# Kernel tuning notes

Measured on AMD Instinct MI355X. Metric: run time of the kernel, lower is better.

The kernel has to match this reference:

```python
import jax, jax.numpy as jnp
import numpy as np

B, Q, L, D = 4, 600, 2048, 256
H, HD, DFF, KD = 8, 32, 2048, 32  # heads, head_dim, ffn dim, gasa kernel dim
SCALE = HD ** -0.5


def setup_inputs() -> dict:
    key = jax.random.key(0)
    ks = jax.random.split(key, 24)
    w = lambda k, shape, s=0.02: (jax.random.normal(k, shape, jnp.float32) * s)
    inp = {
        "queries": jax.random.normal(ks[0], (B, Q, D), jnp.float32),
        "memory": jax.random.normal(ks[1], (B, L, D), jnp.float32),
        "memory_pos": jax.random.normal(ks[2], (B, L, 3), jnp.float32),
        "query_pos": jax.random.normal(ks[3], (B, Q, 3), jnp.float32),
        # self-attention (nn.MultiheadAttention packed in_proj)
        "sa_in_w": w(ks[4], (3 * D, D)), "sa_in_b": jnp.zeros((3 * D,), jnp.float32),
        "sa_out_w": w(ks[5], (D, D)), "sa_out_b": jnp.zeros((D,), jnp.float32),
        "norm1_g": jnp.ones((D,), jnp.float32), "norm1_b": jnp.zeros((D,), jnp.float32),
        # cross-attention projections
        "q_w": w(ks[6], (D, D)), "q_b": jnp.zeros((D,), jnp.float32),
        "k_w": w(ks[7], (D, D)), "k_b": jnp.zeros((D,), jnp.float32),
        "v_w": w(ks[8], (D, D)), "v_b": jnp.zeros((D,), jnp.float32),
        "o_w": w(ks[9], (D, D)), "o_b": jnp.zeros((D,), jnp.float32),
        "norm2_g": jnp.ones((D,), jnp.float32), "norm2_b": jnp.zeros((D,), jnp.float32),
        # GASA geometric-bias kernel: beta, MLP 1->KD->1
        "beta": jnp.asarray(1.0, jnp.float32),
        "dk_w1": w(ks[10], (KD, 1), 0.1), "dk_b1": jnp.zeros((KD,), jnp.float32),
        "dk_w2": w(ks[11], (1, KD), 0.1), "dk_b2": jnp.full((1,), -1.0, jnp.float32),
        # FFN
        "ffn_w1": w(ks[12], (DFF, D)), "ffn_b1": jnp.zeros((DFF,), jnp.float32),
        "ffn_w2": w(ks[13], (D, DFF)), "ffn_b2": jnp.zeros((D,), jnp.float32),
        "norm3_g": jnp.ones((D,), jnp.float32), "norm3_b": jnp.zeros((D,), jnp.float32),
    }
    return inp


def _ln(x, g, b, eps=1e-5):
    m = jnp.mean(x, -1, keepdims=True)
    v = jnp.mean((x - m) ** 2, -1, keepdims=True)
    return (x - m) * jax.lax.rsqrt(v + eps) * g + b


def _heads(x, wt, b):  # x:[B,N,D] -> [B,H,N,HD]
    y = x @ wt.T + b
    return y.reshape(x.shape[0], x.shape[1], H, HD).transpose(0, 2, 1, 3)


def reference(queries, memory, memory_pos, query_pos,
              sa_in_w, sa_in_b, sa_out_w, sa_out_b, norm1_g, norm1_b,
              q_w, q_b, k_w, k_b, v_w, v_b, o_w, o_b, norm2_g, norm2_b,
              beta, dk_w1, dk_b1, dk_w2, dk_b2,
              ffn_w1, ffn_b1, ffn_w2, ffn_b2, norm3_g, norm3_b):
    # ---- self-attention (post-norm, no query_pe) ----
    wq, wk, wv = jnp.split(sa_in_w, 3, axis=0)
    bq, bk, bv = jnp.split(sa_in_b, 3)
    qh = _heads(queries, wq, bq)
    kh = _heads(queries, wk, bk)
    vh = _heads(queries, wv, bv)
    a = jax.nn.softmax(jnp.einsum('bhqd,bhkd->bhqk', qh, kh) * SCALE, axis=-1)
    sa = jnp.einsum('bhqk,bhkd->bhqd', a, vh).transpose(0, 2, 1, 3).reshape(B, Q, D)
    sa = sa @ sa_out_w.T + sa_out_b
    x = _ln(queries + sa, norm1_g, norm1_b)

    # ---- GASA cross-attention ----
    Qh = _heads(x, q_w, q_b)          # [B,H,Q,HD]
    Kh = _heads(memory, k_w, k_b)     # [B,H,L,HD]
    Vh = _heads(memory, v_w, v_b)     # [B,H,L,HD]
    # cdist + learned kernel MLP, clamp to [-10, 0] (suppress-only)
    d2 = jnp.sum((query_pos[:, :, None, :] - memory_pos[:, None, :, :]) ** 2, -1)
    dist = jnp.sqrt(jnp.maximum(d2, 0.0))                     # [B,Q,L]
    hid = jax.nn.relu(dist[..., None] * dk_w1[:, 0] + dk_b1)  # [B,Q,L,KD]
    bias = (hid @ dk_w2[0]) + dk_b2[0]                        # [B,Q,L]
    bias = jnp.clip(bias, -10.0, 0.0)
    scores = jnp.einsum('bhqd,bhkd->bhqk', Qh, Kh) * SCALE + beta * bias[:, None]
    attn = jax.nn.softmax(scores, axis=-1)
    ca = jnp.einsum('bhqk,bhkd->bhqd', attn, Vh).transpose(0, 2, 1, 3).reshape(B, Q, D)
    ca = ca @ o_w.T + o_b
    x = _ln(x + ca, norm2_g, norm2_b)

    # ---- FFN (post-norm) ----
    f = jax.nn.relu(x @ ffn_w1.T + ffn_b1) @ ffn_w2.T + ffn_b2
    return _ln(x + f, norm3_g, norm3_b)
```

## Files before the change

### kernel.cpp

```cpp
#include <hip/hip_runtime.h>
#include <hip/hip_bf16.h>

typedef __hip_bfloat16 bf16;
typedef __attribute__((ext_vector_type(8))) short  short8;
typedef __attribute__((ext_vector_type(4))) short  short4v;
typedef __attribute__((ext_vector_type(4))) float  f32x4;

#define B_ 4
#define Q_ 600
#define L_ 2048
#define D_ 256
#define H_ 8
#define HD_ 32
#define DFF_ 2048
#define KD_ 32
#define SCALE_ 0.17677669529663687f
#define L2E_   1.4426950408889634f
#define SL2E_  (SCALE_ * L2E_)

template<int MODE>
__device__ __forceinline__ float ldx(const void* p, size_t i, bool f32)
{
    if (MODE == 0) return __bfloat162float(((const bf16*)p)[i]);
    if (MODE == 1) return ((const float*)p)[i];
    return f32 ? ((const float*)p)[i] : __bfloat162float(((const bf16*)p)[i]);
}
__device__ __forceinline__ short8 ld8_f32(const float* p)
{
    const float4 a = *(const float4*)p;
    const float4 b = *(const float4*)(p + 4);
    union { short8 s; bf16 h[8]; } u;
    u.h[0] = __float2bfloat16(a.x); u.h[1] = __float2bfloat16(a.y);
    u.h[2] = __float2bfloat16(a.z); u.h[3] = __float2bfloat16(a.w);
    u.h[4] = __float2bfloat16(b.x); u.h[5] = __float2bfloat16(b.y);
    u.h[6] = __float2bfloat16(b.z); u.h[7] = __float2bfloat16(b.w);
    return u.s;
}
template<int MODE>
__device__ __forceinline__ short8 ld8x(const void* p, size_t i, bool f32)
{
    if (MODE == 0) return *(const short8*)((const bf16*)p + i);
    if (MODE == 1) return ld8_f32((const float*)p + i);
    return f32 ? ld8_f32((const float*)p + i) : *(const short8*)((const bf16*)p + i);
}

template<int NSEG>
__device__ __forceinline__ short8 ld8_comb(const bf16* __restrict__ pO,
                                           const float* __restrict__ pml,
                                           int row, int col)
{
    const unsigned b = (unsigned)row / 600u;
    const unsigned q = (unsigned)row - b * 600u;
    const int h = col >> 5, dd = col & 31;
    const unsigned rp = b * 4800u + (unsigned)h * 600u + q;
    float W = 0.f;
    float acc[8] = {0.f,0.f,0.f,0.f,0.f,0.f,0.f,0.f};
    #pragma unroll
    for (int s = 0; s < NSEG; s++) {
        const size_t rr = (size_t)s * 19200u + rp;
        const float l = pml[rr * 2 + 1];
        W += l;
        const short8 o = *(const short8*)(pO + rr * 32 + dd);
        #pragma unroll
        for (int j = 0; j < 8; j++)
            acc[j] += l * __bfloat162float(((const bf16*)&o)[j]);
    }
    const float inv = 1.f / W;
    union { short8 s; bf16 h8[8]; } u;
    #pragma unroll
    for (int j = 0; j < 8; j++) u.h8[j] = __float2bfloat16(acc[j] * inv);
    return u.s;
}

__global__ __launch_bounds__(256)
void detect_kernel(const unsigned short* __restrict__ q, int* __restrict__ flag)
{
    __shared__ float red[4];
    const int tid = threadIdx.x;
    unsigned short u = q[tid];
    float f = __uint_as_float(((unsigned)(u & 0x7FFF)) << 16);
    if (f != f) f = 1e30f;
    #pragma unroll
    for (int o = 32; o > 0; o >>= 1) f = fmaxf(f, __shfl_xor(f, o));
    if ((tid & 63) == 0) red[tid >> 6] = f;
    __syncthreads();
    if (tid == 0) {
        float m = fmaxf(fmaxf(red[0], red[1]), fmaxf(red[2], red[3]));
        *flag = (m > 100.f) ? 1 : 0;
    }
}

template<int AM, int NSEG>
__device__ __forceinline__ void gemm_core(const void* __restrict__ A,
    const void* __restrict__ W, int M, int K, int kbeg, int kend,
    int bm, int bn, bool f32, bf16* As, bf16* Bs, f32x4 (&acc)[2][2],
    const float* __restrict__ pml)
{
    const int tid = threadIdx.x;
    const int w = tid >> 6, lane = tid & 63;
    const int quad = lane >> 4, l16 = lane & 15;
    const int wm = (w & 1) << 5, wn = (w >> 1) << 5;
    const int srow = tid >> 2, scol = (tid & 3) << 3;
    const int gma = (bm + srow < M) ? bm + srow : M - 1;

    short8 pa, pb;
    if constexpr (AM == 3) pa = ld8_comb<NSEG>((const bf16*)A, pml, gma, kbeg + scol);
    else                   pa = ld8x<AM>(A, (size_t)gma * K + kbeg + scol, f32);
    pb = ld8x<2>(W, (size_t)(bn + srow) * K + kbeg + scol, f32);

    for (int k0 = kbeg; k0 < kend; k0 += 32) {
        *(short8*)&As[srow * 40 + scol] = pa;
        *(short8*)&Bs[srow * 40 + scol] = pb;
        __syncthreads();
        if (k0 + 32 < kend) {
            if constexpr (AM == 3) pa = ld8_comb<NSEG>((const bf16*)A, pml, gma, k0 + 32 + scol);
            else                   pa = ld8x<AM>(A, (size_t)gma * K + k0 + 32 + scol, f32);
            pb = ld8x<2>(W, (size_t)(bn + srow) * K + k0 + 32 + scol, f32);
        }
        short8 af[2], bfr[2];
        #pragma unroll
        for (int t = 0; t < 2; t++) {
            af[t]  = *(const short8*)&As[(wm + t * 16 + l16) * 40 + quad * 8];
            bfr[t] = *(const short8*)&Bs[(wn + t * 16 + l16) * 40 + quad * 8];
        }
        #pragma unroll
        for (int mt = 0; mt < 2; mt++)
            #pragma unroll
            for (int nt = 0; nt < 2; nt++)
                acc[mt][nt] = __builtin_amdgcn_mfma_f32_16x16x32_bf16(
                    af[mt], bfr[nt], acc[mt][nt], 0, 0, 0);
        __syncthreads();
    }
}

template<int RM, int CM, bool RELU>
__device__ __forceinline__ void gemm_epi(const f32x4 (&acc)[2][2],
    const void* __restrict__ bias, const void* __restrict__ R,
    void* __restrict__ C, int M, int N, int bm, int bn, bool f32)
{
    const int tid = threadIdx.x;
    const int w = tid >> 6, lane = tid & 63;
    const int quad = lane >> 4, l16 = lane & 15;
    const int wm = (w & 1) << 5, wn = (w >> 1) << 5;
    #pragma unroll
    for (int mt = 0; mt < 2; mt++) {
        #pragma unroll
        for (int r = 0; r < 4; r++) {
            const int row = bm + wm + mt * 16 + quad * 4 + r;
            if (row >= M) continue;
            #pragma unroll
            for (int nt = 0; nt < 2; nt++) {
                const int col = bn + wn + nt * 16 + l16;
                float v = acc[mt][nt][r] + ldx<2>(bias, col, f32);
                if (RM >= 0) v += ldx<(RM < 0 ? 0 : RM)>(R, (size_t)row * N + col, f32);
                if (RELU) v = fmaxf(v, 0.f);
                if (CM == 0) ((bf16*)C)[(size_t)row * N + col] = __float2bfloat16(v);
                else         ((float*)C)[(size_t)row * N + col] = v;
            }
        }
    }
}

template<int AM, int RM, int CM, bool RELU, int SPLIT, int NSEG>
__global__ __launch_bounds__(256)
void gemm_mfma(const void* __restrict__ A, const void* __restrict__ W,
               const void* __restrict__ bias, const void* __restrict__ R,
               void* __restrict__ C, int M, int N, int K,
               const int* __restrict__ flagp, const float* __restrict__ pml)
{
    const bool f32 = (*flagp != 0);
    __shared__ alignas(16) bf16 As[64 * 40];
    __shared__ alignas(16) bf16 Bs[64 * 40];
    const int bm = blockIdx.y << 6, bn = blockIdx.x << 6;
    const int KS = K / SPLIT, z = (SPLIT > 1) ? blockIdx.z : 0;

    f32x4 acc[2][2] = {{{0.f,0.f,0.f,0.f},{0.f,0.f,0.f,0.f}},
                       {{0.f,0.f,0.f,0.f},{0.f,0.f,0.f,0.f}}};
    gemm_core<AM, NSEG>(A, W, M, K, z * KS, z * KS + KS, bm, bn, f32, As, Bs, acc, pml);

    if (SPLIT > 1) {
        const int tid = threadIdx.x;
        const int w = tid >> 6, lane = tid & 63;
        const int quad = lane >> 4, l16 = lane & 15;
        const int wm = (w & 1) << 5, wn = (w >> 1) << 5;
        #pragma unroll
        for (int mt = 0; mt < 2; mt++)
            #pragma unroll
            for (int r = 0; r < 4; r++) {
                const int row = bm + wm + mt * 16 + quad * 4 + r;
                if (row >= M) continue;
                #pragma unroll
                for (int nt = 0; nt < 2; nt++) {
                    const int col = bn + wn + nt * 16 + l16;
                    ((float*)C)[((size_t)z * M + row) * N + col] = acc[mt][nt][r];
                }
            }
    } else {
        gemm_epi<RM, CM, RELU>(acc, bias, R, C, M, N, bm, bn, f32);
    }
}

__global__ __launch_bounds__(256)
void kv_proj(const void* __restrict__ A,
             const void* __restrict__ kw, const void* __restrict__ kb,
             const void* __restrict__ vw, const void* __restrict__ vb,
             bf16* __restrict__ kf, bf16* __restrict__ vf,
             int M, int K, const int* __restrict__ flagp)
{
    const bool f32 = (*flagp != 0);
    __shared__ alignas(16) bf16 As[64 * 40];
    __shared__ alignas(16) bf16 Bs[64 * 40];
    const int sel = blockIdx.x >> 2;
    const void* W  = sel ? vw : kw;
    const void* bs = sel ? vb : kb;
    bf16* C        = sel ? vf : kf;
    const int bn = (blockIdx.x & 3) << 6;
    const int bm = blockIdx.y << 6;

    f32x4 acc[2][2] = {{{0.f,0.f,0.f,0.f},{0.f,0.f,0.f,0.f}},
                       {{0.f,0.f,0.f,0.f},{0.f,0.f,0.f,0.f}}};
    gemm_core<2, 1>(A, W, M, K, 0, K, bm, bn, f32, As, Bs, acc, nullptr);
    gemm_epi<-1, 0, false>(acc, bs, nullptr, C, M, 256, bm, bn, f32);
}

__global__ __launch_bounds__(256)
void bias_pre(const void* __restrict__ qp, const void* __restrict__ mp,
              const void* __restrict__ w1, const void* __restrict__ b1,
              const void* __restrict__ w2, const void* __restrict__ b2,
              const void* __restrict__ betap, bf16* __restrict__ out,
              const int* __restrict__ flagp)
{
    const bool f32 = (*flagp != 0);
    __shared__ float sw1[KD_], sb1[KD_], sw2[KD_], scst[2];
    const int tid = threadIdx.x;
    if (tid < KD_) {
        sw1[tid] = ldx<2>(w1, tid, f32);
        sb1[tid] = ldx<2>(b1, tid, f32);
        sw2[tid] = ldx<2>(w2, tid, f32);
    }
    if (tid == 0) { scst[0] = ldx<2>(b2, 0, f32); scst[1] = L2E_ * ldx<2>(betap, 0, f32); }
    __syncthreads();
    const int idx = blockIdx.x * 256 + tid;
    const int q8 = idx % 75;
    const int t2 = idx / 75;
    const int l = t2 % L_, b = t2 / L_;
    const int q0 = q8 * 8;
    const float mx = ldx<2>(mp, (size_t)(b * L_ + l) * 3 + 0, f32);
    const float my = ldx<2>(mp, (size_t)(b * L_ + l) * 3 + 1, f32);
    const float mz = ldx<2>(mp, (size_t)(b * L_ + l) * 3 + 2, f32);
    union { short8 s; bf16 h[8]; } res;
    #pragma unroll
    for (int j = 0; j < 8; j++) {
        const int q = q0 + j;
        float dx = ldx<2>(qp, (size_t)(b * Q_ + q) * 3 + 0, f32) - mx;
        float dy = ldx<2>(qp, (size_t)(b * Q_ + q) * 3 + 1, f32) - my;
        float dz = ldx<2>(qp, (size_t)(b * Q_ + q) * 3 + 2, f32) - mz;
        float dist = sqrtf(dx * dx + dy * dy + dz * dz);
        float acc = scst[0];
        #pragma unroll
        for (int k = 0; k < KD_; k++)
            acc += fmaxf(dist * sw1[k] + sb1[k], 0.f) * sw2[k];
        acc = fminf(fmaxf(acc, -10.f), 0.f);
        res.h[j] = __float2bfloat16(scst[1] * acc);
    }
    *(short8*)(out + ((size_t)(b * L_) + l) * Q_ + q0) = res.s;
}

template<bool HASBIAS, int NSEG>
__global__ __launch_bounds__(256)
void flash_attn(const bf16* __restrict__ Qm, int qs,
                const bf16* __restrict__ Km, int ks,
                const bf16* __restrict__ Vm, int vs,
                const bf16* __restrict__ biasT,
                bf16* __restrict__ pO, float* __restrict__ pml,
                int NQ, int LK)
{
    __shared__ alignas(16) bf16 Ksh[64 * 40];
    __shared__ alignas(16) bf16 Vt[48 * 72];
    __shared__ alignas(16) bf16 Psh[64 * 72];
    __shared__ alignas(16) bf16 Bsh[HASBIAS ? 64 * 72 : 8];

    const int tid = threadIdx.x;
    const int w = tid >> 6, lane = tid & 63;
    const int quad = lane >> 4, l16 = lane & 15;

    const int id = blockIdx.x;
    const int g  = ((id >> 6) << 3) + (id & 7);
    const int h  = (id >> 3) & 7;
    const int qt = g % 10;
    const int zz = g / 10;
    const int b = zz & 3, seg = zz >> 2;
    const int q0 = qt * 64;
    const int segLen = LK / NSEG;
    const int lbeg = seg * segLen, lend = lbeg + segLen;

    for (int i = tid; i < 16 * 72; i += 256) {
        int rr = 32 + i / 72, cc = i % 72;
        Vt[rr * 72 + cc] = __float2bfloat16(rr == 32 ? 1.f : 0.f);
    }

    int qrow = q0 + w * 16 + l16; if (qrow > NQ - 1) qrow = NQ - 1;
    const short8 aq = *(const short8*)(Qm + (size_t)(b * NQ + qrow) * qs + h * HD_ + quad * 8);

    f32x4 O0 = {0.f,0.f,0.f,0.f}, O1 = {0.f,0.f,0.f,0.f}, O2 = {0.f,0.f,0.f,0.f};

    const int srow = tid >> 2, sc4 = tid & 3;
    const int nch = (segLen + 63) >> 6;

    for (int ch = 0; ch < nch; ch++) {
        const int l0 = lbeg + (ch << 6);
        {
            int lg = l0 + srow; if (lg > LK - 1) lg = LK - 1;
            short8 k8 = *(const short8*)(Km + (size_t)(b * LK + lg) * ks + h * HD_ + sc4 * 8);
            *(short8*)&Ksh[srow * 40 + sc4 * 8] = k8;
            short8 v8 = *(const short8*)(Vm + (size_t)(b * LK + lg) * vs + h * HD_ + sc4 * 8);
            const int swc = srow ^ (sc4 * 16);
            #pragma unroll
            for (int j = 0; j < 8; j++)
                Vt[(sc4 * 8 + j) * 72 + swc] = ((const bf16*)&v8)[j];
            if (HASBIAS) {
                #pragma unroll
                for (int rep = 0; rep < 2; rep++) {
                    int chid = tid + rep * 256;
                    int ll = chid >> 3, qc = chid & 7;
                    int qread = q0 + qc * 8;
                    if (qread > NQ - 8) qread = NQ - 8;
                    *(short8*)&Bsh[ll * 72 + qc * 8] =
                        *(const short8*)(biasT + ((size_t)(b * LK) + l0 + ll) * Q_ + qread);
                }
            }
        }
        __syncthreads();

        f32x4 sv[4];
        #pragma unroll
        for (int jt = 0; jt < 4; jt++) {
            short8 kb = *(const short8*)&Ksh[(jt * 16 + l16) * 40 + quad * 8];
            sv[jt] = __builtin_amdgcn_mfma_f32_16x16x32_bf16(aq, kb, (f32x4){0.f,0.f,0.f,0.f}, 0, 0, 0);
        }
        if (l0 + 64 <= lend) {
            #pragma unroll
            for (int jt = 0; jt < 4; jt++) {
                if (HASBIAS) {
                    short4v bb = *(const short4v*)&Bsh[(jt * 16 + l16) * 72 + w * 16 + quad * 4];
                    #pragma unroll
                    for (int r = 0; r < 4; r++)
                        Psh[(w * 16 + quad * 4 + r) * 72 + jt * 16 + l16] =
                            __float2bfloat16(exp2f(sv[jt][r] * SL2E_ +
                                __bfloat162float(((const bf16*)&bb)[r])));
                } else {
                    #pragma unroll
                    for (int r = 0; r < 4; r++)
                        Psh[(w * 16 + quad * 4 + r) * 72 + jt * 16 + l16] =
                            __float2bfloat16(exp2f(sv[jt][r] * SL2E_));
                }
            }
        } else {
            #pragma unroll
            for (int jt = 0; jt < 4; jt++) {
                const bool valid = (l0 + jt * 16 + l16) < lend;
                #pragma unroll
                for (int r = 0; r < 4; r++)
                    Psh[(w * 16 + quad * 4 + r) * 72 + jt * 16 + l16] =
                        __float2bfloat16(valid ? exp2f(sv[jt][r] * SL2E_) : 0.f);
            }
        }
        __syncthreads();
        const int sw0 = 16 * (l16 >> 3);
        const int sw1 = 16 * (2 + (l16 >> 3));
        #pragma unroll
        for (int kt = 0; kt < 2; kt++) {
            short8 ap  = *(const short8*)&Psh[(w * 16 + l16) * 72 + kt * 32 + quad * 8];
            short8 bv0 = *(const short8*)&Vt[(l16) * 72 + ((kt * 32 + quad * 8) ^ sw0)];
            short8 bv1 = *(const short8*)&Vt[(16 + l16) * 72 + ((kt * 32 + quad * 8) ^ sw1)];
            short8 bon = *(const short8*)&Vt[(32 + l16) * 72 + kt * 32 + quad * 8];
            O0 = __builtin_amdgcn_mfma_f32_16x16x32_bf16(ap, bv0, O0, 0, 0, 0);
            O1 = __builtin_amdgcn_mfma_f32_16x16x32_bf16(ap, bv1, O1, 0, 0, 0);
            O2 = __builtin_amdgcn_mfma_f32_16x16x32_bf16(ap, bon, O2, 0, 0, 0);
        }
        __syncthreads();
    }

    #pragma unroll
    for (int r = 0; r < 4; r++) {
        const int qg = q0 + w * 16 + quad * 4 + r;
        if (qg >= NQ) continue;
        const float li = __shfl(O2[r], lane & 48);
        const float inv = 1.f / li;
        const size_t rowp = (size_t)(((seg * 4 + b) * 8) + h) * NQ + qg;
        bf16* op = pO + rowp * 32;
        op[l16]      = __float2bfloat16(O0[r] * inv);
        op[16 + l16] = __float2bfloat16(O1[r] * inv);
        if (l16 == 0) pml[rowp * 2 + 1] = O2[r];
    }
}

template<int RM, int OM, int S>
__global__ __launch_bounds__(64)
void red_ln(const float* __restrict__ P, const void* __restrict__ bias,
            const void* __restrict__ R, const void* __restrict__ gg,
            const void* __restrict__ bb, void* __restrict__ Y,
            int M, const int* __restrict__ flagp)
{
    const bool f32 = (*flagp != 0);
    const int row = blockIdx.x, lane = threadIdx.x;
    const int d0 = lane * 4;
    float v[4];
    {
        float4 a = *(const float4*)(P + ((size_t)0 * M + row) * D_ + d0);
        v[0] = a.x; v[1] = a.y; v[2] = a.z; v[3] = a.w;
    }
    #pragma unroll
    for (int s = 1; s < S; s++) {
        float4 a = *(const float4*)(P + ((size_t)s * M + row) * D_ + d0);
        v[0] += a.x; v[1] += a.y; v[2] += a.z; v[3] += a.w;
    }
    #pragma unroll
    for (int j = 0; j < 4; j++)
        v[j] += ldx<2>(bias, d0 + j, f32) + ldx<RM>(R, (size_t)row * D_ + d0 + j, f32);

    float s1 = v[0] + v[1] + v[2] + v[3];
    float s2 = v[0]*v[0] + v[1]*v[1] + v[2]*v[2] + v[3]*v[3];
    #pragma unroll
    for (int o = 32; o > 0; o >>= 1) {
        s1 += __shfl_xor(s1, o);
        s2 += __shfl_xor(s2, o);
    }
    const float mean = s1 * (1.f / D_);
    const float var = s2 * (1.f / D_) - mean * mean;
    const float rinv = rsqrtf(var + 1e-5f);
    float o[4];
    #pragma unroll
    for (int j = 0; j < 4; j++)
        o[j] = (v[j] - mean) * rinv * ldx<2>(gg, d0 + j, f32) + ldx<2>(bb, d0 + j, f32);
    const size_t i = (size_t)row * D_ + d0;
    if (OM == 1 || (OM == 2 && f32)) {
        float4 t{o[0], o[1], o[2], o[3]};
        *(float4*)((float*)Y + i) = t;
    } else {
        bf16* y = (bf16*)Y + i;
        y[0] = __float2bfloat16(o[0]); y[1] = __float2bfloat16(o[1]);
        y[2] = __float2bfloat16(o[2]); y[3] = __float2bfloat16(o[3]);
    }
}

extern "C" void kernel_launch(void* const* d_in, const int* in_sizes, int n_in,
                              void* d_out, int out_size, void* d_ws, size_t ws_size,
                              hipStream_t stream)
{
    const void* queries   = d_in[0];
    const void* memory    = d_in[1];
    const void* memory_pos= d_in[2];
    const void* query_pos = d_in[3];
    const void* sa_in_w   = d_in[4];
    const void* sa_in_b   = d_in[5];
    const void* sa_out_w  = d_in[6];
    const void* sa_out_b  = d_in[7];
    const void* norm1_g   = d_in[8];
    const void* norm1_b   = d_in[9];
    const void* q_w  = d_in[10], *q_b  = d_in[11];
    const void* k_w  = d_in[12], *k_b  = d_in[13];
    const void* v_w  = d_in[14], *v_b  = d_in[15];
    const void* o_w  = d_in[16], *o_b  = d_in[17];
    const void* norm2_g = d_in[18], *norm2_b = d_in[19];
    const void* beta  = d_in[20];
    const void* dk_w1 = d_in[21], *dk_b1 = d_in[22];
    const void* dk_w2 = d_in[23], *dk_b2 = d_in[24];
    const void* ffn_w1 = d_in[25], *ffn_b1 = d_in[26];
    const void* ffn_w2 = d_in[27], *ffn_b2 = d_in[28];
    const void* norm3_g = d_in[29], *norm3_b = d_in[30];

    char* base = (char*)d_ws;
    bf16*  kf      = (bf16*)(base + 0);
    bf16*  vf      = (bf16*)(base + 4194304);
    bf16*  biasT   = (bf16*)(base + 8388608);
    bf16*  qkv     = (bf16*)(base + 18219008);
    bf16*  selfO   = (bf16*)(base + 21905408);
    float* selfML  = (float*)(base + 24363008);
    float* P3      = (float*)(base + 24670208);
    float* x1      = (float*)(base + 18219008);
    bf16*  qproj   = (bf16*)(base + 20676608);
    bf16*  crossO  = (bf16*)(base + 21905408);
    float* crossML = (float*)(base + 26820608);
    float* P10     = (float*)(base + 0);
    float* x2      = (float*)(base + 4915200);
    bf16*  ffnh    = (bf16*)(base + 7372800);
    float* P13     = (float*)(base + 17203200);
    int*   flag    = (int*)(base + 29585408);

    const dim3 blk(256);

    detect_kernel<<<1, 256, 0, stream>>>((const unsigned short*)queries, flag);
    gemm_mfma<2, -1, 0, false, 1, 1><<<dim3(12, 38), blk, 0, stream>>>(
        queries, sa_in_w, sa_in_b, nullptr, qkv, 2400, 768, 256, flag, nullptr);
    kv_proj<<<dim3(8, 128), blk, 0, stream>>>(
        memory, k_w, k_b, v_w, v_b, kf, vf, 8192, 256, flag);
    bias_pre<<<2400, blk, 0, stream>>>(
        query_pos, memory_pos, dk_w1, dk_b1, dk_w2, dk_b2, beta, biasT, flag);
    flash_attn<false, 2><<<640, blk, 0, stream>>>(
        qkv, 768, qkv + 256, 768, qkv + 512, 768, nullptr,
        selfO, selfML, 600, 600);
    gemm_mfma<3, -1, 1, false, 2, 2><<<dim3(4, 38, 2), blk, 0, stream>>>(
        selfO, sa_out_w, nullptr, nullptr, P3, 2400, 256, 256, flag, selfML);
    red_ln<2, 1, 2><<<2400, 64, 0, stream>>>(
        P3, sa_out_b, queries, norm1_g, norm1_b, x1, 2400, flag);
    gemm_mfma<1, -1, 0, false, 1, 1><<<dim3(4, 38), blk, 0, stream>>>(
        x1, q_w, q_b, nullptr, qproj, 2400, 256, 256, flag, nullptr);
    flash_attn<true, 4><<<1280, blk, 0, stream>>>(
        qproj, 256, kf, 256, vf, 256, biasT,
        crossO, crossML, 600, 2048);
    gemm_mfma<3, -1, 1, false, 2, 4><<<dim3(4, 38, 2), blk, 0, stream>>>(
        crossO, o_w, nullptr, nullptr, P10, 2400, 256, 256, flag, crossML);
    red_ln<1, 1, 2><<<2400, 64, 0, stream>>>(
        P10, o_b, x1, norm2_g, norm2_b, x2, 2400, flag);
    gemm_mfma<1, -1, 0, true, 1, 1><<<dim3(32, 38), blk, 0, stream>>>(
        x2, ffn_w1, ffn_b1, nullptr, ffnh, 2400, 2048, 256, flag, nullptr);
    gemm_mfma<0, -1, 1, false, 4, 1><<<dim3(4, 38, 4), blk, 0, stream>>>(
        ffnh, ffn_w2, nullptr, nullptr, P13, 2400, 256, 2048, flag, nullptr);
    red_ln<1, 2, 4><<<2400, 64, 0, stream>>>(
        P13, ffn_b2, x2, norm3_g, norm3_b, d_out, 2400, flag);
}
```

Measured before the change: 290.1 us.

## Prefetch next K/V/bias chunk into registers, merge QKV and KV projections, use hardware exp2

The flash attention loop now issues the global loads for the next 64-key chunk of K, V and the bias right after the barrier, holding them in registers, so their latency overlaps the current chunk's MFMA and softmax work. The self-attention QKV projection and the memory K/V projection become one launch that picks its GEMM by block index, which saves a launch and fills the GPU more evenly. exp2f is replaced by the raw hardware exp2 builtin, which drops the library's range handling. In exchange the kernel uses more registers and the exponent may be slightly less accurate for extreme inputs.

```diff
diff --git a/kernel.cpp b/kernel.cpp
--- a/kernel.cpp
+++ b/kernel.cpp
@@ -17,6 +17,8 @@
 #define SCALE_ 0.17677669529663687f
 #define L2E_   1.4426950408889634f
 #define SL2E_  (SCALE_ * L2E_)
+
+__device__ __forceinline__ float fexp2(float x) { return __builtin_amdgcn_exp2f(x); }
 
 template<int MODE>
 __device__ __forceinline__ float ldx(const void* p, size_t i, bool f32)
@@ -201,26 +203,40 @@
 }
 
 __global__ __launch_bounds__(256)
-void kv_proj(const void* __restrict__ A,
-             const void* __restrict__ kw, const void* __restrict__ kb,
-             const void* __restrict__ vw, const void* __restrict__ vb,
-             bf16* __restrict__ kf, bf16* __restrict__ vf,
-             int M, int K, const int* __restrict__ flagp)
+void proj3(const void* __restrict__ queries,
+           const void* __restrict__ sa_in_w, const void* __restrict__ sa_in_b,
+           bf16* __restrict__ qkv,
+           const void* __restrict__ memory,
+           const void* __restrict__ kw, const void* __restrict__ kb,
+           const void* __restrict__ vw, const void* __restrict__ vb,
+           bf16* __restrict__ kf, bf16* __restrict__ vf,
+           const int* __restrict__ flagp)
 {
     const bool f32 = (*flagp != 0);
     __shared__ alignas(16) bf16 As[64 * 40];
     __shared__ alignas(16) bf16 Bs[64 * 40];
-    const int sel = blockIdx.x >> 2;
-    const void* W  = sel ? vw : kw;
-    const void* bs = sel ? vb : kb;
-    bf16* C        = sel ? vf : kf;
-    const int bn = (blockIdx.x & 3) << 6;
-    const int bm = blockIdx.y << 6;
+    const int bid = blockIdx.x;
+
+    const void *A, *W, *bsp;
+    void* C;
+    int M, N, bm, bn;
+    if (bid < 456) {
+        A = queries; W = sa_in_w; bsp = sa_in_b; C = qkv;
+        M = 2400; N = 768;
+        bm = (bid / 12) << 6; bn = (bid % 12) << 6;
+    } else {
+        const int id = bid - 456;
+        const int sel = (id & 7) >> 2;
+        A = memory; W = sel ? vw : kw; bsp = sel ? vb : kb;
+        C = sel ? (void*)vf : (void*)kf;
+        M = 8192; N = 256;
+        bm = (id >> 3) << 6; bn = (id & 3) << 6;
+    }
 
     f32x4 acc[2][2] = {{{0.f,0.f,0.f,0.f},{0.f,0.f,0.f,0.f}},
                        {{0.f,0.f,0.f,0.f},{0.f,0.f,0.f,0.f}}};
-    gemm_core<2, 1>(A, W, M, K, 0, K, bm, bn, f32, As, Bs, acc, nullptr);
-    gemm_epi<-1, 0, false>(acc, bs, nullptr, C, M, 256, bm, bn, f32);
+    gemm_core<2, 1>(A, W, M, 256, 0, 256, bm, bn, f32, As, Bs, acc, nullptr);
+    gemm_epi<-1, 0, false>(acc, bsp, nullptr, C, M, N, bm, bn, f32);
 }
 
 __global__ __launch_bounds__(256)
@@ -307,30 +323,43 @@
     const int srow = tid >> 2, sc4 = tid & 3;
     const int nch = (segLen + 63) >> 6;
 
+    const int ll0 = tid >> 3, ll1 = ll0 + 32, qc = tid & 7;
+    int qr = q0 + qc * 8; if (qr > NQ - 8) qr = NQ - 8;
+
+    int lg0 = lbeg + srow; if (lg0 > LK - 1) lg0 = LK - 1;
+    short8 k8 = *(const short8*)(Km + (size_t)(b * LK + lg0) * ks + h * HD_ + sc4 * 8);
+    short8 v8 = *(const short8*)(Vm + (size_t)(b * LK + lg0) * vs + h * HD_ + sc4 * 8);
+    short8 bb0, bb1;
+    if (HASBIAS) {
+        bb0 = *(const short8*)(biasT + ((size_t)(b * LK) + lbeg + ll0) * Q_ + qr);
+        bb1 = *(const short8*)(biasT + ((size_t)(b * LK) + lbeg + ll1) * Q_ + qr);
+    }
+
     for (int ch = 0; ch < nch; ch++) {
         const int l0 = lbeg + (ch << 6);
+        *(short8*)&Ksh[srow * 40 + sc4 * 8] = k8;
         {
-            int lg = l0 + srow; if (lg > LK - 1) lg = LK - 1;
-            short8 k8 = *(const short8*)(Km + (size_t)(b * LK + lg) * ks + h * HD_ + sc4 * 8);
-            *(short8*)&Ksh[srow * 40 + sc4 * 8] = k8;
-            short8 v8 = *(const short8*)(Vm + (size_t)(b * LK + lg) * vs + h * HD_ + sc4 * 8);
             const int swc = srow ^ (sc4 * 16);
             #pragma unroll
             for (int j = 0; j < 8; j++)
                 Vt[(sc4 * 8 + j) * 72 + swc] = ((const bf16*)&v8)[j];
+        }
+        if (HASBIAS) {
+            *(short8*)&Bsh[ll0 * 72 + qc * 8] = bb0;
+            *(short8*)&Bsh[ll1 * 72 + qc * 8] = bb1;
+        }
+        __syncthreads();
+
+        if (ch + 1 < nch) {
+            const int l0n = l0 + 64;
+            int lg = l0n + srow; if (lg > LK - 1) lg = LK - 1;
+            k8 = *(const short8*)(Km + (size_t)(b * LK + lg) * ks + h * HD_ + sc4 * 8);
+            v8 = *(const short8*)(Vm + (size_t)(b * LK + lg) * vs + h * HD_ + sc4 * 8);
             if (HASBIAS) {
-                #pragma unroll
-                for (int rep = 0; rep < 2; rep++) {
-                    int chid = tid + rep * 256;
-                    int ll = chid >> 3, qc = chid & 7;
-                    int qread = q0 + qc * 8;
-                    if (qread > NQ - 8) qread = NQ - 8;
-                    *(short8*)&Bsh[ll * 72 + qc * 8] =
-                        *(const short8*)(biasT + ((size_t)(b * LK) + l0 + ll) * Q_ + qread);
-                }
+                bb0 = *(const short8*)(biasT + ((size_t)(b * LK) + l0n + ll0) * Q_ + qr);
+                bb1 = *(const short8*)(biasT + ((size_t)(b * LK) + l0n + ll1) * Q_ + qr);
             }
         }
-        __syncthreads();
 
         f32x4 sv[4];
         #pragma unroll
@@ -346,13 +375,13 @@
                     #pragma unroll
                     for (int r = 0; r < 4; r++)
                         Psh[(w * 16 + quad * 4 + r) * 72 + jt * 16 + l16] =
-                            __float2bfloat16(exp2f(sv[jt][r] * SL2E_ +
+                            __float2bfloat16(fexp2(sv[jt][r] * SL2E_ +
                                 __bfloat162float(((const bf16*)&bb)[r])));
                 } else {
                     #pragma unroll
                     for (int r = 0; r < 4; r++)
                         Psh[(w * 16 + quad * 4 + r) * 72 + jt * 16 + l16] =
-                            __float2bfloat16(exp2f(sv[jt][r] * SL2E_));
+                            __float2bfloat16(fexp2(sv[jt][r] * SL2E_));
                 }
             }
         } else {
@@ -362,7 +391,7 @@
                 #pragma unroll
                 for (int r = 0; r < 4; r++)
                     Psh[(w * 16 + quad * 4 + r) * 72 + jt * 16 + l16] =
-                        __float2bfloat16(valid ? exp2f(sv[jt][r] * SL2E_) : 0.f);
+                        __float2bfloat16(valid ? fexp2(sv[jt][r] * SL2E_) : 0.f);
             }
         }
         __syncthreads();
@@ -491,10 +520,9 @@
     const dim3 blk(256);
 
     detect_kernel<<<1, 256, 0, stream>>>((const unsigned short*)queries, flag);
-    gemm_mfma<2, -1, 0, false, 1, 1><<<dim3(12, 38), blk, 0, stream>>>(
-        queries, sa_in_w, sa_in_b, nullptr, qkv, 2400, 768, 256, flag, nullptr);
-    kv_proj<<<dim3(8, 128), blk, 0, stream>>>(
-        memory, k_w, k_b, v_w, v_b, kf, vf, 8192, 256, flag);
+    proj3<<<1480, blk, 0, stream>>>(
+        queries, sa_in_w, sa_in_b, qkv,
+        memory, k_w, k_b, v_w, v_b, kf, vf, flag);
     bias_pre<<<2400, blk, 0, stream>>>(
         query_pos, memory_pos, dk_w1, dk_b1, dk_w2, dk_b2, beta, biasT, flag);
     flash_attn<false, 2><<<640, blk, 0, stream>>>(
```

Result: faster. 279.9 us (-3.5%).
